# Performance work log

Hardware: AMD Instinct MI355X
Metric: run time of the kernel (lower is better)

The kernel has to match this reference:

```python
import jax, jax.numpy as jnp
import numpy as np

G = 128            # grid_size (hardcoded in NeRFRenderer.__init__)
T = 32             # time_size (reduced from 64 to keep working set < 4GB)
CAS = 1            # cascade = 1 + ceil(log2(bound)), bound = 1
DECAY = 0.95
DENSITY_SCALE = 1.0
DENSITY_THRESH = 0.01


def _expand_bits(v):
    # instant-ngp style 10-bit -> 30-bit expansion (works for 7-bit coords of G=128)
    v = (v * jnp.uint32(0x00010001)) & jnp.uint32(0xFF0000FF)
    v = (v * jnp.uint32(0x00000101)) & jnp.uint32(0x0F00F00F)
    v = (v * jnp.uint32(0x00000011)) & jnp.uint32(0xC30C30C3)
    v = (v * jnp.uint32(0x00000005)) & jnp.uint32(0x49249249)
    return v


def _morton3d(coords):
    # coords: [N, 3] int32 in [0, G)
    x = _expand_bits(coords[:, 0].astype(jnp.uint32))
    y = _expand_bits(coords[:, 1].astype(jnp.uint32))
    z = _expand_bits(coords[:, 2].astype(jnp.uint32))
    return (x | (y << 1) | (z << 2)).astype(jnp.int32)


def setup_inputs() -> dict:
    key = jax.random.key(0)
    k1, k2 = jax.random.split(key)
    density_grid = jax.random.normal(k1, (T, CAS, G ** 3), dtype=jnp.float32) * 0.5
    sigmas = jax.random.uniform(k2, (T, CAS, G ** 3), dtype=jnp.float32)
    return {"density_grid": density_grid, "sigmas": sigmas}


def reference(density_grid, sigmas):
    # full-grid branch of update_extra_state (iter_density < 16)
    g = jnp.arange(G, dtype=jnp.int32)
    xx, yy, zz = jnp.meshgrid(g, g, g, indexing='ij')
    coords = jnp.stack([xx.ravel(), yy.ravel(), zz.ravel()], axis=-1)  # [G^3, 3]
    indices = _morton3d(coords)                                        # [G^3]

    # tmp_grid = -1; tmp_grid[t, cas, indices] = sigmas * density_scale
    tmp_grid = -jnp.ones_like(density_grid)
    tmp_grid = tmp_grid.at[:, :, indices].set(sigmas * DENSITY_SCALE)

    # decay / max merge on mutually-valid cells
    valid = (density_grid >= 0) & (tmp_grid >= 0)
    new_grid = jnp.where(valid, jnp.maximum(density_grid * DECAY, tmp_grid), density_grid)

    # threshold + packbits into bitfield (8 cells per byte, morton order)
    mean_density = jnp.mean(jnp.clip(new_grid, 0.0))
    thresh = jnp.minimum(mean_density, jnp.float32(DENSITY_THRESH))
    bits = (new_grid > thresh).reshape(T, -1, 8)                       # [T, CAS*G^3/8, 8]
    weights = (jnp.int32(1) << jnp.arange(8, dtype=jnp.int32))
    bitfield = jnp.sum(bits.astype(jnp.int32) * weights, axis=-1)      # [T, CAS*G^3/8]
    return new_grid, bitfield
```

## Files before the change

### kernel.cpp

```cpp
#include <hip/hip_runtime.h>

#define G    128
#define G3   (G * G * G)
#define TDIM 32
#define NTOT (TDIM * G3)
#define NBYTES_OUT (NTOT / 8)
#define DECAY 0.95f
#define DTH   0.01f
#define NBLK  (TDIM * 256)

typedef float f32x4 __attribute__((ext_vector_type(4)));
typedef float f32x2 __attribute__((ext_vector_type(2)));

__device__ __forceinline__ unsigned expand3(unsigned v) {
    v = (v * 0x00010001u) & 0xFF0000FFu;
    v = (v * 0x00000101u) & 0x0F00F00Fu;
    v = (v * 0x00000011u) & 0xC30C30C3u;
    v = (v * 0x00000005u) & 0x49249249u;
    return v;
}
__device__ __forceinline__ unsigned compact3(unsigned v) {
    v &= 0x49249249u;
    v = (v | (v >> 2))  & 0xC30C30C3u;
    v = (v | (v >> 4))  & 0x0F00F00Fu;
    v = (v | (v >> 8))  & 0xFF0000FFu;
    v = (v | (v >> 16)) & 0x000003FFu;
    return v;
}
__device__ __forceinline__ int swz(int m) {
    return (((m >> 7) & 1) << 2) ^ (((m >> 8) & 1) << 3) ^ (((m >> 10) & 1) << 4);
}

__device__ __forceinline__ f32x4 merge4(f32x4 v, f32x4 s) {
    f32x4 r;
    r.x = (v.x >= 0.f && s.x >= 0.f) ? fmaxf(v.x * DECAY, s.x) : v.x;
    r.y = (v.y >= 0.f && s.y >= 0.f) ? fmaxf(v.y * DECAY, s.y) : v.y;
    r.z = (v.z >= 0.f && s.z >= 0.f) ? fmaxf(v.z * DECAY, s.z) : v.z;
    r.w = (v.w >= 0.f && s.w >= 0.f) ? fmaxf(v.w * DECAY, s.w) : v.w;
    return r;
}

__global__ __launch_bounds__(512, 8) void
pass1(const float* __restrict__ dg, const float* __restrict__ sg,
      float* __restrict__ out_grid, float* __restrict__ out_bits,
      float* __restrict__ partials)
{
    __shared__ float smem[8192];
    __shared__ float wsum[8];
    const int blk  = blockIdx.x;
    const int t    = blk >> 8;
    const int pp   = blk & 255;
    const int c0   = ((pp >> 2) << 3) | (pp & 3);
    const int base = t * G3;
    const int tid  = threadIdx.x;

    const int cu   = tid >> 8;
    const int off  = (tid & 255) << 4;
    const int cube = c0 | (cu << 2);
    const int jg0  = base + (cube << 12) + off;

    const f32x4* dgp = reinterpret_cast<const f32x4*>(dg + jg0);
    const f32x4 v0 = dgp[0];
    const f32x4 v1 = dgp[1];
    const f32x4 v2 = dgp[2];
    const f32x4 v3 = dgp[3];

    const unsigned Xc = compact3((unsigned)c0);
    const unsigned Yc = compact3((unsigned)c0 >> 1);
    const unsigned Zc = compact3((unsigned)c0 >> 2);
    const float* __restrict__ sgt = sg + base + (int)((Xc << 18) | (Yc << 11) | (Zc << 4));
    #pragma unroll
    for (int k = 0; k < 4; ++k) {
        const int c   = tid + (k << 9);
        const int lx  = c >> 7;
        const int ly  = (c >> 3) & 15;
        const int lz  = (c & 7) << 2;
        const f32x4 s = *reinterpret_cast<const f32x4*>(sgt + (lx << 14) + (ly << 7) + lz);
        const int cs  = (lz >> 4) << 12;
        const int m   = (int)(expand3((unsigned)lx) | (expand3((unsigned)ly) << 1)
                            | (expand3((unsigned)(lz & 15)) << 2));
        const int mb  = cs + (m ^ swz(m));
        smem[mb]      = s.x;
        smem[mb ^ 4]  = s.y;
        smem[mb ^ 32] = s.z;
        smem[mb ^ 36] = s.w;
    }
    __syncthreads();

    const int b = (cu << 12) + (off ^ swz(off));
    const f32x4 s0 = *reinterpret_cast<const f32x4*>(&smem[b]);
    const f32x4 s1 = *reinterpret_cast<const f32x4*>(&smem[b ^ 4]);
    const f32x4 s2 = *reinterpret_cast<const f32x4*>(&smem[b ^ 8]);
    const f32x4 s3 = *reinterpret_cast<const f32x4*>(&smem[b ^ 12]);

    const f32x4 r0 = merge4(v0, s0);
    const f32x4 r1 = merge4(v1, s1);
    const f32x4 r2 = merge4(v2, s2);
    const f32x4 r3 = merge4(v3, s3);

    f32x4* ogp = reinterpret_cast<f32x4*>(out_grid + jg0);
    ogp[0] = r0;
    ogp[1] = r1;
    ogp[2] = r2;
    ogp[3] = r3;

    float lsum = fmaxf(r0.x, 0.f) + fmaxf(r0.y, 0.f) + fmaxf(r0.z, 0.f) + fmaxf(r0.w, 0.f)
               + fmaxf(r1.x, 0.f) + fmaxf(r1.y, 0.f) + fmaxf(r1.z, 0.f) + fmaxf(r1.w, 0.f)
               + fmaxf(r2.x, 0.f) + fmaxf(r2.y, 0.f) + fmaxf(r2.z, 0.f) + fmaxf(r2.w, 0.f)
               + fmaxf(r3.x, 0.f) + fmaxf(r3.y, 0.f) + fmaxf(r3.z, 0.f) + fmaxf(r3.w, 0.f);

    const int byte0 = (r0.x > DTH ? 1 : 0)  | (r0.y > DTH ? 2 : 0)  |
                      (r0.z > DTH ? 4 : 0)  | (r0.w > DTH ? 8 : 0)  |
                      (r1.x > DTH ? 16 : 0) | (r1.y > DTH ? 32 : 0) |
                      (r1.z > DTH ? 64 : 0) | (r1.w > DTH ? 128 : 0);
    const int byte1 = (r2.x > DTH ? 1 : 0)  | (r2.y > DTH ? 2 : 0)  |
                      (r2.z > DTH ? 4 : 0)  | (r2.w > DTH ? 8 : 0)  |
                      (r3.x > DTH ? 16 : 0) | (r3.y > DTH ? 32 : 0) |
                      (r3.z > DTH ? 64 : 0) | (r3.w > DTH ? 128 : 0);
    f32x2 bb; bb.x = (float)byte0; bb.y = (float)byte1;
    *reinterpret_cast<f32x2*>(out_bits + (jg0 >> 3)) = bb;

    #pragma unroll
    for (int offl = 32; offl; offl >>= 1) lsum += __shfl_down(lsum, offl, 64);
    if ((tid & 63) == 0) wsum[tid >> 6] = lsum;
    __syncthreads();
    if (tid == 0) {
        float tot = 0.f;
        #pragma unroll
        for (int i = 0; i < 8; ++i) tot += wsum[i];
        partials[blk] = tot;
    }
}

__global__ __launch_bounds__(1024) void
reduce_thresh(const float* __restrict__ partials, float* __restrict__ thresh)
{
    float s = 0.f;
    for (int i = threadIdx.x; i < NBLK; i += 1024) s += partials[i];
    #pragma unroll
    for (int off = 32; off; off >>= 1) s += __shfl_down(s, off, 64);
    __shared__ float wsum[16];
    if ((threadIdx.x & 63) == 0) wsum[threadIdx.x >> 6] = s;
    __syncthreads();
    if (threadIdx.x == 0) {
        float tot = 0.f;
        #pragma unroll
        for (int i = 0; i < 16; ++i) tot += wsum[i];
        thresh[0] = fminf(tot / (float)NTOT, DTH);
    }
}

__global__ __launch_bounds__(256) void
fix_bits(const float* __restrict__ grid, const float* __restrict__ thresh,
         float* __restrict__ out_bits)
{
    const float th = thresh[0];
    if (th == DTH) return;
    for (int n = blockIdx.x * 256 + threadIdx.x; n < NBYTES_OUT; n += 256 * 1024) {
        const float4* g = reinterpret_cast<const float4*>(grid) + (n << 1);
        const float4 a = g[0], b = g[1];
        int byte = (a.x > th ? 1 : 0)   | (a.y > th ? 2 : 0)   |
                   (a.z > th ? 4 : 0)   | (a.w > th ? 8 : 0)   |
                   (b.x > th ? 16 : 0)  | (b.y > th ? 32 : 0)  |
                   (b.z > th ? 64 : 0)  | (b.w > th ? 128 : 0);
        out_bits[n] = (float)byte;
    }
}

extern "C" void kernel_launch(void* const* d_in, const int* in_sizes, int n_in,
                              void* d_out, int out_size, void* d_ws, size_t ws_size,
                              hipStream_t stream)
{
    const float* dg = (const float*)d_in[0];
    const float* sg = (const float*)d_in[1];
    float* out_grid = (float*)d_out;
    float* out_bits = out_grid + NTOT;
    float* partials = (float*)d_ws;
    float* thresh   = partials + NBLK;

    pass1<<<NBLK, 512, 0, stream>>>(dg, sg, out_grid, out_bits, partials);
    reduce_thresh<<<1, 1024, 0, stream>>>(partials, thresh);
    fix_bits<<<1024, 256, 0, stream>>>(out_grid, thresh, out_bits);
}
```

Before: 165.8 us.

## Retile pass1 blocks as x-y slabs with contiguous sigma reads and f32x4 smem writes

Each block now covers a 16x... slab defined by (sx, sy) so that sigma rows are read as long contiguous chunks and written to shared memory as whole float4s through a new XOR swizzle. The transpose to Morton order moves to the read side, which now does eight f32x2 shared-memory gathers per thread. The goal is more coalesced global sigma loads and fewer scalar LDS stores. In exchange it adds more LDS read instructions, and the changed block-to-grid mapping may alter density_grid access locality.

Measured after the change: 160.8 us. 1.03x faster.

```diff
diff --git a/kernel.cpp b/kernel.cpp
--- a/kernel.cpp
+++ b/kernel.cpp
@@ -19,16 +19,9 @@
     v = (v * 0x00000005u) & 0x49249249u;
     return v;
 }
-__device__ __forceinline__ unsigned compact3(unsigned v) {
-    v &= 0x49249249u;
-    v = (v | (v >> 2))  & 0xC30C30C3u;
-    v = (v | (v >> 4))  & 0x0F00F00Fu;
-    v = (v | (v >> 8))  & 0xFF0000FFu;
-    v = (v | (v >> 16)) & 0x000003FFu;
-    return v;
-}
-__device__ __forceinline__ int swz(int m) {
-    return (((m >> 7) & 1) << 2) ^ (((m >> 8) & 1) << 3) ^ (((m >> 10) & 1) << 4);
+
+__device__ __forceinline__ int swz(int f) {
+    return f ^ ((((f >> 12) & 1) << 3) ^ (((f >> 8) & 1) << 4));
 }
 
 __device__ __forceinline__ f32x4 merge4(f32x4 v, f32x4 s) {
@@ -50,14 +43,15 @@
     const int blk  = blockIdx.x;
     const int t    = blk >> 8;
     const int pp   = blk & 255;
-    const int c0   = ((pp >> 2) << 3) | (pp & 3);
+    const int sx   = pp & 15;
+    const int sy   = pp >> 4;
     const int base = t * G3;
     const int tid  = threadIdx.x;
 
-    const int cu   = tid >> 8;
-    const int off  = (tid & 255) << 4;
-    const int cube = c0 | (cu << 2);
-    const int jg0  = base + (cube << 12) + off;
+    const int m_fixed = (int)((expand3((unsigned)sx) << 9) | (expand3((unsigned)sy) << 10));
+    const int r   = tid >> 5;
+    const int o   = (tid & 31) << 4;
+    const int jg0 = base + m_fixed + (int)(expand3((unsigned)r) << 11) + o;
 
     const f32x4* dgp = reinterpret_cast<const f32x4*>(dg + jg0);
     const f32x4 v0 = dgp[0];
@@ -65,33 +59,42 @@
     const f32x4 v2 = dgp[2];
     const f32x4 v3 = dgp[3];
 
-    const unsigned Xc = compact3((unsigned)c0);
-    const unsigned Yc = compact3((unsigned)c0 >> 1);
-    const unsigned Zc = compact3((unsigned)c0 >> 2);
-    const float* __restrict__ sgt = sg + base + (int)((Xc << 18) | (Yc << 11) | (Zc << 4));
+    const float* __restrict__ sgt = sg + base + (sx << 17) + (sy << 10);
     #pragma unroll
     for (int k = 0; k < 4; ++k) {
         const int c   = tid + (k << 9);
-        const int lx  = c >> 7;
-        const int ly  = (c >> 3) & 15;
-        const int lz  = (c & 7) << 2;
-        const f32x4 s = *reinterpret_cast<const f32x4*>(sgt + (lx << 14) + (ly << 7) + lz);
-        const int cs  = (lz >> 4) << 12;
-        const int m   = (int)(expand3((unsigned)lx) | (expand3((unsigned)ly) << 1)
-                            | (expand3((unsigned)(lz & 15)) << 2));
-        const int mb  = cs + (m ^ swz(m));
-        smem[mb]      = s.x;
-        smem[mb ^ 4]  = s.y;
-        smem[mb ^ 32] = s.z;
-        smem[mb ^ 36] = s.w;
+        const int x   = c >> 8;
+        const int rem = c & 255;
+        const f32x4 s = *reinterpret_cast<const f32x4*>(sgt + (x << 14) + (rem << 2));
+        *reinterpret_cast<f32x4*>(&smem[swz((x << 10) + (rem << 2))]) = s;
     }
     __syncthreads();
 
-    const int b = (cu << 12) + (off ^ swz(off));
-    const f32x4 s0 = *reinterpret_cast<const f32x4*>(&smem[b]);
-    const f32x4 s1 = *reinterpret_cast<const f32x4*>(&smem[b ^ 4]);
-    const f32x4 s2 = *reinterpret_cast<const f32x4*>(&smem[b ^ 8]);
-    const f32x4 s3 = *reinterpret_cast<const f32x4*>(&smem[b ^ 12]);
+    const int lb = tid & 31;
+    const int y1 = lb & 1, z1 = (lb >> 1) & 1, x2 = (lb >> 2) & 1;
+    const int y2 = (lb >> 3) & 1, z2 = (lb >> 4) & 1;
+    const int zz = (z1 << 1) + (z2 << 2) + (r << 3);
+
+    f32x2 p0, p1, p2, p3, p4, p5, p6, p7;
+    {
+        const int xA = 2 * 0 + 4 * x2;
+        const int xB = 2 * 1 + 4 * x2;
+        const int yA = 2 * y1 + 4 * y2;
+        const int fA = (xA << 10) + (yA << 7) + zz;
+        const int fB = (xB << 10) + (yA << 7) + zz;
+        p0 = *reinterpret_cast<const f32x2*>(&smem[swz(fA)]);
+        p1 = *reinterpret_cast<const f32x2*>(&smem[swz(fA + 1024)]);
+        p2 = *reinterpret_cast<const f32x2*>(&smem[swz(fA + 128)]);
+        p3 = *reinterpret_cast<const f32x2*>(&smem[swz(fA + 1152)]);
+        p4 = *reinterpret_cast<const f32x2*>(&smem[swz(fB)]);
+        p5 = *reinterpret_cast<const f32x2*>(&smem[swz(fB + 1024)]);
+        p6 = *reinterpret_cast<const f32x2*>(&smem[swz(fB + 128)]);
+        p7 = *reinterpret_cast<const f32x2*>(&smem[swz(fB + 1152)]);
+    }
+    f32x4 s0; s0.x = p0.x; s0.y = p1.x; s0.z = p2.x; s0.w = p3.x;
+    f32x4 s1; s1.x = p0.y; s1.y = p1.y; s1.z = p2.y; s1.w = p3.y;
+    f32x4 s2; s2.x = p4.x; s2.y = p5.x; s2.z = p6.x; s2.w = p7.x;
+    f32x4 s3; s3.x = p4.y; s3.y = p5.y; s3.z = p6.y; s3.w = p7.y;
 
     const f32x4 r0 = merge4(v0, s0);
     const f32x4 r1 = merge4(v1, s1);
```
